# Kernel optimization log

Hardware: AMD Instinct MI355X
Metric: run time of the kernel (lower is better)

Reference implementation:

```python
import jax, jax.numpy as jnp
import numpy as np

HEAD_DIM = 128
HIDDEN = 5120
NUM_KV_GROUPS = 8
NUM_MODALITIES = 3
NUM_Q_HEADS = 40
QKV_PER_MOD = NUM_Q_HEADS * HEAD_DIM + 2 * NUM_KV_GROUPS * HEAD_DIM + NUM_Q_HEADS  # 7208


def _rms_norm(x, w, eps=1e-6):
    xf = x.astype(jnp.float32)
    inv = jax.lax.rsqrt(jnp.mean(xf * xf, axis=-1, keepdims=True) + eps)
    return (xf * inv).astype(x.dtype) * w


def _apply_rope(x, cos, sin):
    # x: [B,S,H,D], cos/sin: [B,S,rd]
    rd = cos.shape[-1]
    xr, xp = x[..., :rd], x[..., rd:]
    c, s = cos[:, :, None, :], sin[:, :, None, :]
    x1, x2 = xr[..., : rd // 2], xr[..., rd // 2:]
    rot = jnp.concatenate([-x2, x1], axis=-1)
    return jnp.concatenate([xr * c + rot * s, xp], axis=-1)


def setup_inputs() -> dict:
    key = jax.random.key(0)
    ks = jax.random.split(key, 6)
    B, S = 1, 2048
    return {
        "x": jax.random.normal(ks[0], (B, S, HIDDEN), jnp.float32),
        "rope_cos": jax.random.uniform(ks[1], (B, S, HEAD_DIM), jnp.float32),
        "rope_sin": jax.random.uniform(ks[2], (B, S, HEAD_DIM), jnp.float32),
        "modality_ids": jax.random.randint(ks[3], (B, S), 0, NUM_MODALITIES, jnp.int32),
        "pre_norm": jnp.ones((NUM_MODALITIES * HIDDEN,), jnp.float32),
        "qkv_w": jax.random.normal(ks[4], (NUM_MODALITIES * QKV_PER_MOD, HIDDEN), jnp.float32) * 0.02,
        "q_norm": jnp.ones((NUM_MODALITIES * HEAD_DIM,), jnp.float32),
        "k_norm": jnp.ones((NUM_MODALITIES * HEAD_DIM,), jnp.float32),
        "proj_w": jax.random.normal(ks[5], (NUM_MODALITIES * HIDDEN, HIDDEN), jnp.float32) * 0.02,
    }


def reference(x, rope_cos, rope_sin, modality_ids, pre_norm, qkv_w, q_norm, k_norm, proj_w):
    B, S, _ = x.shape
    # per-token modality gather of pre-norm weight
    norm_w = pre_norm.reshape(NUM_MODALITIES, HIDDEN)[modality_ids]  # [B,S,H]
    normed = _rms_norm(x, norm_w)

    # modality-routed QKV: compute all modalities, select with one-hot (dense, jit-friendly)
    oh = jax.nn.one_hot(modality_ids, NUM_MODALITIES, dtype=x.dtype)  # [B,S,M]
    qkv_w3 = qkv_w.reshape(NUM_MODALITIES, QKV_PER_MOD, HIDDEN)
    qkv_all = jnp.einsum("bsh,moh->bsmo", normed, qkv_w3)  # [B,S,M,QKV]
    qkv = jnp.einsum("bsm,bsmo->bso", oh, qkv_all)

    q_dim = NUM_Q_HEADS * HEAD_DIM
    k_dim = NUM_KV_GROUPS * HEAD_DIM
    q = qkv[..., :q_dim].reshape(B, S, NUM_Q_HEADS, HEAD_DIM)
    k = qkv[..., q_dim:q_dim + k_dim].reshape(B, S, NUM_KV_GROUPS, HEAD_DIM)
    v = qkv[..., q_dim + k_dim:q_dim + 2 * k_dim].reshape(B, S, NUM_KV_GROUPS, HEAD_DIM)
    gate = jax.nn.sigmoid(qkv[..., q_dim + 2 * k_dim:q_dim + 2 * k_dim + NUM_Q_HEADS])  # [B,S,NQ]

    qn = q_norm.reshape(NUM_MODALITIES, HEAD_DIM)[modality_ids][:, :, None, :]  # [B,S,1,D]
    kn = k_norm.reshape(NUM_MODALITIES, HEAD_DIM)[modality_ids][:, :, None, :]
    q = _rms_norm(q, qn)
    k = _rms_norm(k, kn)

    q = _apply_rope(q, rope_cos, rope_sin)
    k = _apply_rope(k, rope_cos, rope_sin)

    repeat = NUM_Q_HEADS // NUM_KV_GROUPS
    k = jnp.repeat(k, repeat, axis=2)  # [B,S,NQ,D]
    v = jnp.repeat(v, repeat, axis=2)

    scale = 1.0 / np.sqrt(HEAD_DIM)
    scores = jnp.einsum("bqhd,bkhd->bhqk", q, k) * scale  # [B,NQ,S,S]
    attn = jax.nn.softmax(scores, axis=-1)
    out = jnp.einsum("bhqk,bkhd->bqhd", attn, v)  # [B,S,NQ,D]

    out = (out * gate[..., None]).reshape(B, S, NUM_Q_HEADS * HEAD_DIM)

    proj_w3 = proj_w.reshape(NUM_MODALITIES, HIDDEN, HIDDEN)
    proj_all = jnp.einsum("bsh,moh->bsmo", out, proj_w3)  # [B,S,M,H]
    return jnp.einsum("bsm,bsmo->bso", oh, proj_all)
```

## Files before the change

### kernel.cpp

```cpp
#include <hip/hip_runtime.h>

typedef _Float16 f16;
typedef f16 f16x8 __attribute__((ext_vector_type(8)));
typedef f16 f16x4 __attribute__((ext_vector_type(4)));
typedef float f32x4 __attribute__((ext_vector_type(4)));

#define HID 5120
#define QKVO 7208
#define S_TOK 2048
#define NQH 40
#define NKV 8
#define HD 128

__device__ __forceinline__ void gload16(const void* g, void* l) {
    __builtin_amdgcn_global_load_lds(
        (const __attribute__((address_space(1))) void*)g,
        (__attribute__((address_space(3))) void*)l,
        16, 0, 0);
}

__global__ void sort_tokens(const int* __restrict__ mod, int* __restrict__ sorted,
                            int* __restrict__ offs)
{
    int tid = threadIdx.x, wave = tid >> 6, lane = tid & 63;
    int mloc[8];
    int c[3] = {0, 0, 0};
#pragma unroll
    for (int j = 0; j < 8; ++j) {
        int m = mod[tid * 8 + j];
        mloc[j] = m;
        c[m]++;
    }
    __shared__ int wsum[4][3];
    int excl[3];
#pragma unroll
    for (int m = 0; m < 3; ++m) {
        int v = c[m];
        int incl = v;
        for (int d = 1; d < 64; d <<= 1) {
            int n = __shfl_up(incl, d, 64);
            if (lane >= d) incl += n;
        }
        excl[m] = incl - v;
        if (lane == 63) wsum[wave][m] = incl;
    }
    __syncthreads();
    int wbase[3], tot[3];
#pragma unroll
    for (int m = 0; m < 3; ++m) {
        int b = 0, t = 0;
        for (int w = 0; w < 4; ++w) {
            if (w < wave) b += wsum[w][m];
            t += wsum[w][m];
        }
        wbase[m] = b;
        tot[m] = t;
    }
    int base[3];
    base[0] = 0;
    base[1] = tot[0];
    base[2] = tot[0] + tot[1];
    if (tid == 0) {
        offs[0] = 0;
        offs[1] = tot[0];
        offs[2] = tot[0] + tot[1];
        offs[3] = S_TOK;
    }
    int pos[3];
#pragma unroll
    for (int m = 0; m < 3; ++m) pos[m] = base[m] + wbase[m] + excl[m];
#pragma unroll
    for (int j = 0; j < 8; ++j) {
        int m = mloc[j];
        sorted[pos[m]++] = tid * 8 + j;
    }
}

__global__ void cvt_f32_f16(const float* __restrict__ src, f16* __restrict__ dst, int n4)
{
    int i = blockIdx.x * 256 + threadIdx.x;
    int stride = gridDim.x * 256;
    const float4* s4 = (const float4*)src;
    f16x4* d4 = (f16x4*)dst;
    for (; i < n4; i += stride) {
        float4 a = s4[i];
        f16x4 h;
        h[0] = (f16)a.x; h[1] = (f16)a.y; h[2] = (f16)a.z; h[3] = (f16)a.w;
        d4[i] = h;
    }
}

__global__ void rms_pre(const float* __restrict__ x, const int* __restrict__ mod,
                        const float* __restrict__ prenorm, f16* __restrict__ A1)
{
    int tok = blockIdx.x, tid = threadIdx.x;
    int m = mod[tok];
    const float4* xv = (const float4*)(x + (size_t)tok * HID);
    float4 v[5];
    float ss = 0.f;
#pragma unroll
    for (int j = 0; j < 5; ++j) {
        v[j] = xv[tid + 256 * j];
        ss += v[j].x * v[j].x + v[j].y * v[j].y + v[j].z * v[j].z + v[j].w * v[j].w;
    }
    for (int d = 1; d < 64; d <<= 1) ss += __shfl_xor(ss, d, 64);
    __shared__ float ws[4];
    if ((tid & 63) == 0) ws[tid >> 6] = ss;
    __syncthreads();
    float tot = ws[0] + ws[1] + ws[2] + ws[3];
    float inv = rsqrtf(tot * (1.f / HID) + 1e-6f);
    const float4* wv = (const float4*)(prenorm + (size_t)m * HID);
    f16x4* out4 = (f16x4*)(A1 + (size_t)tok * HID);
#pragma unroll
    for (int j = 0; j < 5; ++j) {
        float4 w = wv[tid + 256 * j];
        f16x4 h;
        h[0] = (f16)(v[j].x * inv * w.x);
        h[1] = (f16)(v[j].y * inv * w.y);
        h[2] = (f16)(v[j].z * inv * w.z);
        h[3] = (f16)(v[j].w * inv * w.w);
        out4[tid + 256 * j] = h;
    }
}

__global__ void gemm_grouped(const f16* __restrict__ A, const f16* __restrict__ W,
                             float* __restrict__ C,
                             const int* __restrict__ sorted_tok,
                             const int* __restrict__ mod_off, int NW, int NTN, int NPAN)
{
    const int K = HID;
    int F = blockIdx.x;
    int g = F & 7, s = F >> 3;
    int P = (s >> 4) * 8 + g;
    if (P >= NPAN) return;
    int mt = s & 15;
    int nt = P % NTN, mod = P / NTN;
    int off = mod_off[mod], cnt = mod_off[mod + 1] - off;
    if (mt * 128 >= cnt) return;
    __shared__ __align__(16) f16 As[128 * 64];
    __shared__ __align__(16) f16 Bs[128 * 64];
    __shared__ int rowtok[128];
    int tid = threadIdx.x, wave = tid >> 6, lane = tid & 63;
    if (tid < 128) {
        int r = mt * 128 + tid;
        rowtok[tid] = (r < cnt) ? sorted_tok[off + r] : -1;
    }
    __syncthreads();
    int wr = wave >> 1, wc = wave & 1;
    f32x4 acc[4][4] = {};
    const f16* Wm = W + (size_t)mod * NW * K;
    for (int kt = 0; kt < K / 64; ++kt) {
        int k0 = kt * 64;
#pragma unroll
        for (int it = 0; it < 4; ++it) {
            int c = it * 256 + tid;
            int row = c >> 3, kc = c & 7, skc = kc ^ (row & 7);
            int tk = rowtok[row];
            if (tk < 0) tk = 0;
            gload16(A + (size_t)tk * K + k0 + skc * 8, &As[c * 8]);
        }
#pragma unroll
        for (int it = 0; it < 4; ++it) {
            int c = it * 256 + tid;
            int row = c >> 3, kc = c & 7, skc = kc ^ (row & 7);
            int o = nt * 128 + row;
            if (o >= NW) o = NW - 1;
            gload16(Wm + (size_t)o * K + k0 + skc * 8, &Bs[c * 8]);
        }
        __syncthreads();
#pragma unroll
        for (int ks = 0; ks < 2; ++ks) {
            f16x8 a[4], b[4];
#pragma unroll
            for (int i = 0; i < 4; ++i) {
                int ar = wr * 64 + i * 16 + (lane & 15);
                int ac = (ks * 4 + (lane >> 4)) ^ (ar & 7);
                a[i] = *(const f16x8*)&As[ar * 64 + ac * 8];
                int br = wc * 64 + i * 16 + (lane & 15);
                int bc = (ks * 4 + (lane >> 4)) ^ (br & 7);
                b[i] = *(const f16x8*)&Bs[br * 64 + bc * 8];
            }
#pragma unroll
            for (int mi = 0; mi < 4; ++mi)
#pragma unroll
                for (int nj = 0; nj < 4; ++nj)
                    acc[mi][nj] = __builtin_amdgcn_mfma_f32_16x16x32_f16(
                        a[mi], b[nj], acc[mi][nj], 0, 0, 0);
        }
        __syncthreads();
    }
    int cl = lane & 15, rg = lane >> 4;
#pragma unroll
    for (int mi = 0; mi < 4; ++mi) {
#pragma unroll
        for (int rr = 0; rr < 4; ++rr) {
            int row = wr * 64 + mi * 16 + rg * 4 + rr;
            int tk = rowtok[row];
            if (tk < 0) continue;
            float* crow = C + (size_t)tk * NW;
#pragma unroll
            for (int nj = 0; nj < 4; ++nj) {
                int o = nt * 128 + wc * 64 + nj * 16 + cl;
                if (o < NW) crow[o] = acc[mi][nj][rr];
            }
        }
    }
}

__global__ void qkv_post(const float* __restrict__ qkv, const int* __restrict__ mod,
                         const float* __restrict__ cosb, const float* __restrict__ sinb,
                         const float* __restrict__ qnorm, const float* __restrict__ knorm,
                         f16* __restrict__ Qb, f16* __restrict__ Kb, float* __restrict__ gateb)
{
    int tok = blockIdx.x, tid = threadIdx.x;
    int wave = tid >> 6, lane = tid & 63;
    int m = mod[tok];
    float c0 = cosb[tok * HD + lane], c1 = cosb[tok * HD + 64 + lane];
    float s0 = sinb[tok * HD + lane], s1 = sinb[tok * HD + 64 + lane];
    const float* row = qkv + (size_t)tok * QKVO;
    for (int u = wave; u < 48; u += 4) {
        int base = (u < 40) ? u * HD : NQH * HD + (u - 40) * HD;
        float x0 = row[base + lane];
        float x1 = row[base + 64 + lane];
        float ss = x0 * x0 + x1 * x1;
        for (int d = 1; d < 64; d <<= 1) ss += __shfl_xor(ss, d, 64);
        float inv = rsqrtf(ss * (1.f / HD) + 1e-6f);
        const float* nw = (u < 40 ? qnorm : knorm) + m * HD;
        float n0 = x0 * inv * nw[lane];
        float n1 = x1 * inv * nw[64 + lane];
        float r0 = n0 * c0 - n1 * s0;
        float r1 = n1 * c1 + n0 * s1;
        if (u < 40) {
            const float sc = 0.08838834764831845f;
            r0 *= sc; r1 *= sc;
            Qb[((size_t)u * S_TOK + tok) * HD + lane] = (f16)r0;
            Qb[((size_t)u * S_TOK + tok) * HD + 64 + lane] = (f16)r1;
        } else {
            Kb[((size_t)(u - 40) * S_TOK + tok) * HD + lane] = (f16)r0;
            Kb[((size_t)(u - 40) * S_TOK + tok) * HD + 64 + lane] = (f16)r1;
        }
    }
    if (tid < 40) {
        float g = row[NQH * HD + 2 * NKV * HD + tid];
        gateb[tok * 40 + tid] = 1.f / (1.f + __expf(-g));
    }
}

__global__ void vtrans(const float* __restrict__ qkv, f16* __restrict__ Vt)
{
    int tc = blockIdx.x;
    int g = blockIdx.y;
    int tid = threadIdx.x;
    __shared__ float tile[64][129];
#pragma unroll
    for (int it = 0; it < 8; ++it) {
        int idx = it * 256 + tid;
        int r = idx >> 5, c4 = idx & 31;
        float4 v = *(const float4*)(qkv + (size_t)(tc * 64 + r) * QKVO + NQH * HD + NKV * HD + g * HD + c4 * 4);
        tile[r][c4 * 4 + 0] = v.x;
        tile[r][c4 * 4 + 1] = v.y;
        tile[r][c4 * 4 + 2] = v.z;
        tile[r][c4 * 4 + 3] = v.w;
    }
    __syncthreads();
    int d = tid >> 1, half = tid & 1;
    f16* dst = Vt + ((size_t)g * HD + d) * S_TOK + tc * 64 + half * 32;
#pragma unroll
    for (int j = 0; j < 32; ++j) dst[j] = (f16)tile[half * 32 + j][d];
}

__global__ void attn(const f16* __restrict__ Qb, const f16* __restrict__ Kb,
                     const f16* __restrict__ Vtb, const float* __restrict__ gateb,
                     f16* __restrict__ A2)
{
    int qt = blockIdx.x, h = blockIdx.y, grp = h / 5;
    int tid = threadIdx.x, wave = tid >> 6, lane = tid & 63;
    __shared__ __align__(16) char smem[73728];
    f16* Qs  = (f16*)smem;
    f16* Kb0 = (f16*)(smem + 16384);
    f16* Kb1 = (f16*)smem;
    f16* Vb0 = (f16*)(smem + 32768);
    f16* Vb1 = (f16*)(smem + 49152);
    char* pbase = smem + 65536 + wave * 2048;

    const f16* Qg = Qb + ((size_t)h * S_TOK + qt * 64) * HD;
    const f16* Kg = Kb + (size_t)grp * S_TOK * HD;
    const f16* Vg = Vtb + (size_t)grp * HD * S_TOK;

#pragma unroll
    for (int it = 0; it < 4; ++it) {
        int c = it * 256 + tid, row = c >> 4, kc = c & 15, skc = kc ^ (row & 15);
        gload16(Qg + row * HD + skc * 8, &Qs[c * 8]);
    }
#pragma unroll
    for (int it = 0; it < 4; ++it) {
        int c = it * 256 + tid, row = c >> 4, kc = c & 15, skc = kc ^ (row & 15);
        gload16(Kg + (size_t)row * HD + skc * 8, &Kb0[c * 8]);
    }
#pragma unroll
    for (int it = 0; it < 4; ++it) {
        int c = it * 256 + tid, row = c >> 3, kc = c & 7, skc = kc ^ (row & 7);
        gload16(Vg + (size_t)row * S_TOK + skc * 8, &Vb0[c * 8]);
    }
    asm volatile("s_waitcnt vmcnt(8)" ::: "memory");
    __builtin_amdgcn_s_barrier();
    f16x8 qf[4];
    {
        int row = wave * 16 + (lane & 15);
#pragma unroll
        for (int ks = 0; ks < 4; ++ks) {
            int sk = (ks * 4 + (lane >> 4)) ^ (row & 15);
            qf[ks] = *(const f16x8*)&Qs[row * 128 + sk * 8];
        }
    }
    asm volatile("s_waitcnt lgkmcnt(0)" ::: "memory");
    __builtin_amdgcn_s_barrier();

    f32x4 o[8] = {};
    float mrow[4] = {-3.0e38f, -3.0e38f, -3.0e38f, -3.0e38f};
    float lrow[4] = {0.f, 0.f, 0.f, 0.f};

    int cur = 0;
    for (int t = 0; t < 32; ++t) {
        f16* Ks = cur ? Kb1 : Kb0;
        f16* Vs = cur ? Vb1 : Vb0;
        if (t < 31) {
            f16* Kn = cur ? Kb0 : Kb1;
            f16* Vn = cur ? Vb0 : Vb1;
#pragma unroll
            for (int it = 0; it < 4; ++it) {
                int c = it * 256 + tid, row = c >> 4, kc = c & 15, skc = kc ^ (row & 15);
                gload16(Kg + (size_t)((t + 1) * 64 + row) * HD + skc * 8, &Kn[c * 8]);
            }
#pragma unroll
            for (int it = 0; it < 4; ++it) {
                int c = it * 256 + tid, row = c >> 3, kc = c & 7, skc = kc ^ (row & 7);
                gload16(Vg + (size_t)row * S_TOK + (t + 1) * 64 + skc * 8, &Vn[c * 8]);
            }
            asm volatile("s_waitcnt vmcnt(8)" ::: "memory");
        } else {
            asm volatile("s_waitcnt vmcnt(0)" ::: "memory");
        }
        __builtin_amdgcn_s_barrier();

        f32x4 s[4] = {};
#pragma unroll
        for (int ks = 0; ks < 4; ++ks) {
#pragma unroll
            for (int nj = 0; nj < 4; ++nj) {
                int kr = nj * 16 + (lane & 15);
                int sk = (ks * 4 + (lane >> 4)) ^ (kr & 15);
                f16x8 kf = *(const f16x8*)&Ks[kr * 128 + sk * 8];
                s[nj] = __builtin_amdgcn_mfma_f32_16x16x32_f16(qf[ks], kf, s[nj], 0, 0, 0);
            }
        }
        float mx[4], corr[4], psum[4];
#pragma unroll
        for (int r = 0; r < 4; ++r)
            mx[r] = fmaxf(fmaxf(s[0][r], s[1][r]), fmaxf(s[2][r], s[3][r]));
        for (int d = 1; d < 16; d <<= 1) {
#pragma unroll
            for (int r = 0; r < 4; ++r) mx[r] = fmaxf(mx[r], __shfl_xor(mx[r], d, 16));
        }
#pragma unroll
        for (int r = 0; r < 4; ++r) {
            float mn = fmaxf(mrow[r], mx[r]);
            corr[r] = __expf(mrow[r] - mn);
            mrow[r] = mn;
            psum[r] = 0.f;
        }
#pragma unroll
        for (int nj = 0; nj < 4; ++nj) {
#pragma unroll
            for (int r = 0; r < 4; ++r) {
                float p = __expf(s[nj][r] - mrow[r]);
                psum[r] += p;
                int prow = (lane >> 4) * 4 + r, col = (lane & 15) + nj * 16;
                int addr = (prow * 128 + col * 2) ^ ((prow & 7) << 4);
                *(f16*)(pbase + addr) = (f16)p;
            }
        }
        for (int d = 1; d < 16; d <<= 1) {
#pragma unroll
            for (int r = 0; r < 4; ++r) psum[r] += __shfl_xor(psum[r], d, 16);
        }
#pragma unroll
        for (int r = 0; r < 4; ++r) lrow[r] = lrow[r] * corr[r] + psum[r];
#pragma unroll
        for (int nj2 = 0; nj2 < 8; ++nj2)
#pragma unroll
            for (int r = 0; r < 4; ++r) o[nj2][r] *= corr[r];
#pragma unroll
        for (int ks2 = 0; ks2 < 2; ++ks2) {
            int prow = lane & 15;
            int sk = (ks2 * 4 + (lane >> 4)) ^ (prow & 7);
            f16x8 pa = *(const f16x8*)(pbase + prow * 128 + sk * 16);
#pragma unroll
            for (int nj2 = 0; nj2 < 8; ++nj2) {
                int vr = nj2 * 16 + (lane & 15);
                int skv = (ks2 * 4 + (lane >> 4)) ^ (vr & 7);
                f16x8 vf = *(const f16x8*)&Vs[vr * 64 + skv * 8];
                o[nj2] = __builtin_amdgcn_mfma_f32_16x16x32_f16(pa, vf, o[nj2], 0, 0, 0);
            }
        }
        asm volatile("s_waitcnt lgkmcnt(0)" ::: "memory");
        __builtin_amdgcn_s_barrier();
        cur ^= 1;
    }
    int rbase = qt * 64 + wave * 16 + (lane >> 4) * 4;
#pragma unroll
    for (int r = 0; r < 4; ++r) {
        int tok = rbase + r;
        float sc = gateb[tok * 40 + h] / lrow[r];
#pragma unroll
        for (int nj2 = 0; nj2 < 8; ++nj2) {
            int d = nj2 * 16 + (lane & 15);
            A2[(size_t)tok * HID + h * HD + d] = (f16)(o[nj2][r] * sc);
        }
    }
}

extern "C" void kernel_launch(void* const* d_in, const int* in_sizes, int n_in,
                              void* d_out, int out_size, void* d_ws, size_t ws_size,
                              hipStream_t stream)
{
    const float* x = (const float*)d_in[0];
    const float* rc = (const float*)d_in[1];
    const float* rs = (const float*)d_in[2];
    const int* mod = (const int*)d_in[3];
    const float* prenorm = (const float*)d_in[4];
    const float* qkvw = (const float*)d_in[5];
    const float* qn = (const float*)d_in[6];
    const float* kn = (const float*)d_in[7];
    const float* projw = (const float*)d_in[8];
    float* out = (float*)d_out;

    char* p = (char*)d_ws;
    auto alloc = [&](size_t bytes) {
        char* r = p;
        p += (bytes + 255) & ~(size_t)255;
        return r;
    };
    int* sorted = (int*)alloc(S_TOK * 4);
    int* offs = (int*)alloc(16);
    f16* A1 = (f16*)alloc((size_t)S_TOK * HID * 2);
    f16* Wq = (f16*)alloc((size_t)3 * QKVO * HID * 2);
    f16* Wp = (f16*)alloc((size_t)3 * HID * HID * 2);
    float* qkv = (float*)alloc((size_t)S_TOK * QKVO * 4);
    f16* Qb = (f16*)alloc((size_t)NQH * S_TOK * HD * 2);
    f16* Kb = (f16*)alloc((size_t)NKV * S_TOK * HD * 2);
    f16* Vt = (f16*)alloc((size_t)NKV * HD * S_TOK * 2);
    float* gate = (float*)alloc((size_t)S_TOK * 40 * 4);
    f16* A2 = (f16*)alloc((size_t)S_TOK * HID * 2);
    if ((size_t)(p - (char*)d_ws) > ws_size) return;

    sort_tokens<<<1, 256, 0, stream>>>(mod, sorted, offs);
    cvt_f32_f16<<<2048, 256, 0, stream>>>(qkvw, Wq, 3 * QKVO * HID / 4);
    cvt_f32_f16<<<2048, 256, 0, stream>>>(projw, Wp, 3 * HID * HID / 4);
    rms_pre<<<2048, 256, 0, stream>>>(x, mod, prenorm, A1);
    {
        int NTN = 57, NPAN = NTN * 3;
        int grid = 8 * ((NPAN + 7) / 8) * 16;
        gemm_grouped<<<grid, 256, 0, stream>>>(A1, Wq, qkv, sorted, offs, QKVO, NTN, NPAN);
    }
    qkv_post<<<2048, 256, 0, stream>>>(qkv, mod, rc, rs, qn, kn, Qb, Kb, gate);
    vtrans<<<dim3(32, 8), 256, 0, stream>>>(qkv, Vt);
    attn<<<dim3(32, 40), 256, 0, stream>>>(Qb, Kb, Vt, gate, A2);
    {
        int NTN = 40, NPAN = NTN * 3;
        int grid = 8 * ((NPAN + 7) / 8) * 16;
        gemm_grouped<<<grid, 256, 0, stream>>>(A2, Wp, out, sorted, offs, HID, NTN, NPAN);
    }
}
```

Measured before the change: 914.0 us.

## Enlarge attention tile to 128 queries with lazy rescale and packed P stores

The attention kernel now runs 512 threads covering 128 query rows per block, so each K/V tile loaded into shared memory is reused by twice as many waves. The online softmax only rescales the accumulators when the running max grows by more than 8, and softmax probabilities are written to LDS as packed 4-wide vectors instead of scalar stores. It also raises wave priority around the MFMA sections and permutes the V transpose column order so the packed P layout matches. The extra shared memory and larger blocks may reduce occupancy, and the lazy rescale relies on bounded score growth to stay accurate.

```diff
diff --git a/kernel.cpp b/kernel.cpp
--- a/kernel.cpp
+++ b/kernel.cpp
@@ -264,45 +264,49 @@
     }
     __syncthreads();
     int d = tid >> 1, half = tid & 1;
-    f16* dst = Vt + ((size_t)g * HD + d) * S_TOK + tc * 64 + half * 32;
-#pragma unroll
-    for (int j = 0; j < 32; ++j) dst[j] = (f16)tile[half * 32 + j][d];
-}
-
-__global__ void attn(const f16* __restrict__ Qb, const f16* __restrict__ Kb,
-                     const f16* __restrict__ Vtb, const float* __restrict__ gateb,
-                     f16* __restrict__ A2)
+    f16* dst = Vt + ((size_t)g * HD + d) * S_TOK + tc * 64;
+#pragma unroll
+    for (int j = 0; j < 32; ++j) {
+        int c = half * 32 + j;
+        dst[c] = (f16)tile[16 * (c & 3) + (c >> 2)][d];
+    }
+}
+
+__global__ __launch_bounds__(512, 4) void attn(
+    const f16* __restrict__ Qb, const f16* __restrict__ Kb,
+    const f16* __restrict__ Vtb, const float* __restrict__ gateb,
+    f16* __restrict__ A2)
 {
     int qt = blockIdx.x, h = blockIdx.y, grp = h / 5;
     int tid = threadIdx.x, wave = tid >> 6, lane = tid & 63;
-    __shared__ __align__(16) char smem[73728];
+    __shared__ __align__(16) char smem[81920];
     f16* Qs  = (f16*)smem;
-    f16* Kb0 = (f16*)(smem + 16384);
     f16* Kb1 = (f16*)smem;
-    f16* Vb0 = (f16*)(smem + 32768);
-    f16* Vb1 = (f16*)(smem + 49152);
-    char* pbase = smem + 65536 + wave * 2048;
-
-    const f16* Qg = Qb + ((size_t)h * S_TOK + qt * 64) * HD;
+    char* pbase = smem + 16384 + wave * 2048;
+    f16* Kb0 = (f16*)(smem + 32768);
+    f16* Vb0 = (f16*)(smem + 49152);
+    f16* Vb1 = (f16*)(smem + 65536);
+
+    const f16* Qg = Qb + ((size_t)h * S_TOK + qt * 128) * HD;
     const f16* Kg = Kb + (size_t)grp * S_TOK * HD;
     const f16* Vg = Vtb + (size_t)grp * HD * S_TOK;
 
 #pragma unroll
     for (int it = 0; it < 4; ++it) {
-        int c = it * 256 + tid, row = c >> 4, kc = c & 15, skc = kc ^ (row & 15);
+        int c = it * 512 + tid, row = c >> 4, kc = c & 15, skc = kc ^ (row & 15);
         gload16(Qg + row * HD + skc * 8, &Qs[c * 8]);
     }
 #pragma unroll
-    for (int it = 0; it < 4; ++it) {
-        int c = it * 256 + tid, row = c >> 4, kc = c & 15, skc = kc ^ (row & 15);
+    for (int it = 0; it < 2; ++it) {
+        int c = it * 512 + tid, row = c >> 4, kc = c & 15, skc = kc ^ (row & 15);
         gload16(Kg + (size_t)row * HD + skc * 8, &Kb0[c * 8]);
     }
 #pragma unroll
-    for (int it = 0; it < 4; ++it) {
-        int c = it * 256 + tid, row = c >> 3, kc = c & 7, skc = kc ^ (row & 7);
+    for (int it = 0; it < 2; ++it) {
+        int c = it * 512 + tid, row = c >> 3, kc = c & 7, skc = kc ^ (row & 7);
         gload16(Vg + (size_t)row * S_TOK + skc * 8, &Vb0[c * 8]);
     }
-    asm volatile("s_waitcnt vmcnt(8)" ::: "memory");
+    asm volatile("s_waitcnt vmcnt(4)" ::: "memory");
     __builtin_amdgcn_s_barrier();
     f16x8 qf[4];
     {
@@ -328,22 +332,23 @@
             f16* Kn = cur ? Kb0 : Kb1;
             f16* Vn = cur ? Vb0 : Vb1;
 #pragma unroll
-            for (int it = 0; it < 4; ++it) {
-                int c = it * 256 + tid, row = c >> 4, kc = c & 15, skc = kc ^ (row & 15);
+            for (int it = 0; it < 2; ++it) {
+                int c = it * 512 + tid, row = c >> 4, kc = c & 15, skc = kc ^ (row & 15);
                 gload16(Kg + (size_t)((t + 1) * 64 + row) * HD + skc * 8, &Kn[c * 8]);
             }
 #pragma unroll
-            for (int it = 0; it < 4; ++it) {
-                int c = it * 256 + tid, row = c >> 3, kc = c & 7, skc = kc ^ (row & 7);
+            for (int it = 0; it < 2; ++it) {
+                int c = it * 512 + tid, row = c >> 3, kc = c & 7, skc = kc ^ (row & 7);
                 gload16(Vg + (size_t)row * S_TOK + (t + 1) * 64 + skc * 8, &Vn[c * 8]);
             }
-            asm volatile("s_waitcnt vmcnt(8)" ::: "memory");
+            asm volatile("s_waitcnt vmcnt(4)" ::: "memory");
         } else {
             asm volatile("s_waitcnt vmcnt(0)" ::: "memory");
         }
         __builtin_amdgcn_s_barrier();
 
         f32x4 s[4] = {};
+        __builtin_amdgcn_s_setprio(1);
 #pragma unroll
         for (int ks = 0; ks < 4; ++ks) {
 #pragma unroll
@@ -354,7 +359,8 @@
                 s[nj] = __builtin_amdgcn_mfma_f32_16x16x32_f16(qf[ks], kf, s[nj], 0, 0, 0);
             }
         }
-        float mx[4], corr[4], psum[4];
+        __builtin_amdgcn_s_setprio(0);
+        float mx[4], psum[4];
 #pragma unroll
         for (int r = 0; r < 4; ++r)
             mx[r] = fmaxf(fmaxf(s[0][r], s[1][r]), fmaxf(s[2][r], s[3][r]));
@@ -362,34 +368,42 @@
 #pragma unroll
             for (int r = 0; r < 4; ++r) mx[r] = fmaxf(mx[r], __shfl_xor(mx[r], d, 16));
         }
+        bool need = false;
+#pragma unroll
+        for (int r = 0; r < 4; ++r) need = need || (mx[r] > mrow[r] + 8.f);
+        if (__any(need)) {
+#pragma unroll
+            for (int r = 0; r < 4; ++r) {
+                float nm = fmaxf(mrow[r], mx[r]);
+                float corr = __expf(mrow[r] - nm);
+                mrow[r] = nm;
+                lrow[r] *= corr;
+#pragma unroll
+                for (int nj2 = 0; nj2 < 8; ++nj2) o[nj2][r] *= corr;
+            }
+        }
+#pragma unroll
+        for (int r = 0; r < 4; ++r) psum[r] = 0.f;
 #pragma unroll
         for (int r = 0; r < 4; ++r) {
-            float mn = fmaxf(mrow[r], mx[r]);
-            corr[r] = __expf(mrow[r] - mn);
-            mrow[r] = mn;
-            psum[r] = 0.f;
-        }
-#pragma unroll
-        for (int nj = 0; nj < 4; ++nj) {
-#pragma unroll
-            for (int r = 0; r < 4; ++r) {
+            f16x4 hp;
+#pragma unroll
+            for (int nj = 0; nj < 4; ++nj) {
                 float p = __expf(s[nj][r] - mrow[r]);
                 psum[r] += p;
-                int prow = (lane >> 4) * 4 + r, col = (lane & 15) + nj * 16;
-                int addr = (prow * 128 + col * 2) ^ ((prow & 7) << 4);
-                *(f16*)(pbase + addr) = (f16)p;
-            }
+                hp[nj] = (f16)p;
+            }
+            int q = (lane >> 4) * 4 + r;
+            int addr = q * 128 + ((8 * (lane & 15)) ^ ((q & 7) << 4));
+            *(f16x4*)(pbase + addr) = hp;
         }
         for (int d = 1; d < 16; d <<= 1) {
 #pragma unroll
             for (int r = 0; r < 4; ++r) psum[r] += __shfl_xor(psum[r], d, 16);
         }
 #pragma unroll
-        for (int r = 0; r < 4; ++r) lrow[r] = lrow[r] * corr[r] + psum[r];
-#pragma unroll
-        for (int nj2 = 0; nj2 < 8; ++nj2)
-#pragma unroll
-            for (int r = 0; r < 4; ++r) o[nj2][r] *= corr[r];
+        for (int r = 0; r < 4; ++r) lrow[r] += psum[r];
+        __builtin_amdgcn_s_setprio(1);
 #pragma unroll
         for (int ks2 = 0; ks2 < 2; ++ks2) {
             int prow = lane & 15;
@@ -403,11 +417,12 @@
                 o[nj2] = __builtin_amdgcn_mfma_f32_16x16x32_f16(pa, vf, o[nj2], 0, 0, 0);
             }
         }
+        __builtin_amdgcn_s_setprio(0);
         asm volatile("s_waitcnt lgkmcnt(0)" ::: "memory");
         __builtin_amdgcn_s_barrier();
         cur ^= 1;
     }
-    int rbase = qt * 64 + wave * 16 + (lane >> 4) * 4;
+    int rbase = qt * 128 + wave * 16 + (lane >> 4) * 4;
 #pragma unroll
     for (int r = 0; r < 4; ++r) {
         int tok = rbase + r;
@@ -465,7 +480,7 @@
     }
     qkv_post<<<2048, 256, 0, stream>>>(qkv, mod, rc, rs, qn, kn, Qb, Kb, gate);
     vtrans<<<dim3(32, 8), 256, 0, stream>>>(qkv, Vt);
-    attn<<<dim3(32, 40), 256, 0, stream>>>(Qb, Kb, Vt, gate, A2);
+    attn<<<dim3(16, 40), 512, 0, stream>>>(Qb, Kb, Vt, gate, A2);
     {
         int NTN = 40, NPAN = NTN * 3;
         int grid = 8 * ((NPAN + 7) / 8) * 16;
```

Result: faster. 834.1 us (-8.7%).
